# Kernel tuning notes

Measured on AMD Instinct MI355X. Metric: run time of the kernel, lower is better.

Reference implementation:

```python
import jax, jax.numpy as jnp
import numpy as np

B, T, D, H = 2, 2048, 2048, 16
HD = D // H
EPS = 1e-8
NEG = -1e9


def setup_inputs() -> dict:
    key = jax.random.key(0)
    ks = jax.random.split(key, 6)
    x = jax.random.normal(ks[0], (B, T, D), dtype=jnp.float32)
    # additive causal mask, broadcast over [B, H, T, T]
    causal = jnp.tril(jnp.ones((T, T), dtype=bool))
    attn_mask = jnp.where(causal, 0.0, NEG).astype(jnp.float32)[None, None]
    s = 1.0 / np.sqrt(D)
    w_norm = jnp.ones((D,), dtype=jnp.float32)
    wq = jax.random.normal(ks[1], (D, D), dtype=jnp.float32) * s
    wk = jax.random.normal(ks[2], (D, D), dtype=jnp.float32) * s
    wv = jax.random.normal(ks[3], (D, D), dtype=jnp.float32) * s
    wo = jax.random.normal(ks[4], (D, D), dtype=jnp.float32) * s
    return {"x": x, "attn_mask": attn_mask, "w_norm": w_norm,
            "wq": wq, "wk": wk, "wv": wv, "wo": wo}


def _rmsnorm(x, w):
    # norm = ||x||_2 * D^-0.5 ; out = w * x / (norm + eps)  (eps outside, as in source)
    norm = jnp.sqrt(jnp.sum(x * x, axis=-1, keepdims=True)) * (x.shape[-1] ** -0.5)
    return w * x / (norm + EPS)


def reference(x, attn_mask, w_norm, wq, wk, wv, wo):
    b, t, d = x.shape
    xn = _rmsnorm(x, w_norm)
    # Linear (no bias): y = x @ W^T ; split into heads -> [B, H, T, HD]
    def proj(w):
        return jnp.einsum('btd,ed->bte', xn, w).reshape(b, t, H, HD).transpose(0, 2, 1, 3)
    q, k, v = proj(wq), proj(wk), proj(wv)
    scale = HD ** -0.5
    w_scores = jnp.einsum('bhqd,bhkd->bhqk', q, k) * scale + attn_mask
    p = jax.nn.softmax(w_scores, axis=-1)
    out = jnp.einsum('bhqk,bhkd->bhqd', p, v)
    out = out.transpose(0, 2, 1, 3).reshape(b, t, d)
    return jnp.einsum('btd,ed->bte', out, wo)
```

## Files before the change

### kernel.cpp

```cpp
#include <hip/hip_runtime.h>
#include <stdint.h>

#define TT 2048
#define DD 2048
#define NHH 16
#define HDD 128
#define BTT 4096

typedef __attribute__((ext_vector_type(8))) short bf16x8;
typedef __attribute__((ext_vector_type(4))) float f32x4;

#define MF(a, b, c) __builtin_amdgcn_mfma_f32_16x16x32_bf16(a, b, c, 0, 0, 0)

__device__ __forceinline__ unsigned short f2bf(float f) {
    union { float f; uint32_t u; } v; v.f = f;
    uint32_t u = v.u;
    u += 0x7fffu + ((u >> 16) & 1u);
    return (unsigned short)(u >> 16);
}

__device__ __forceinline__ void gld16(const unsigned short* g, unsigned short* l) {
    __builtin_amdgcn_global_load_lds(
        (const __attribute__((address_space(1))) unsigned int*)g,
        (__attribute__((address_space(3))) unsigned int*)l, 16, 0, 0);
}

__global__ __launch_bounds__(256) void convert_w(const float* __restrict__ wq,
                                                 const float* __restrict__ wk,
                                                 const float* __restrict__ wv,
                                                 const float* __restrict__ wo,
                                                 unsigned short* __restrict__ out) {
    size_t gid = (size_t)blockIdx.x * 256 + threadIdx.x;
    size_t base = gid * 8;
    int which = (int)(base >> 22);
    const float* src = which == 0 ? wq : which == 1 ? wk : which == 2 ? wv : wo;
    size_t off = base & 4194303u;
    float4 a = ((const float4*)(src + off))[0];
    float4 b = ((const float4*)(src + off))[1];
    union { unsigned short us[8]; uint4 v; } pk;
    pk.us[0] = f2bf(a.x); pk.us[1] = f2bf(a.y); pk.us[2] = f2bf(a.z); pk.us[3] = f2bf(a.w);
    pk.us[4] = f2bf(b.x); pk.us[5] = f2bf(b.y); pk.us[6] = f2bf(b.z); pk.us[7] = f2bf(b.w);
    *(uint4*)(out + base) = pk.v;
}

__global__ __launch_bounds__(256) void rmsnorm_k(const float* __restrict__ x,
                                                 const float* __restrict__ w,
                                                 unsigned short* __restrict__ xn) {
    const int row = blockIdx.x;
    const int tid = threadIdx.x;
    const float* xr = x + (size_t)row * DD;
    float4 a = ((const float4*)xr)[tid * 2];
    float4 b = ((const float4*)xr)[tid * 2 + 1];
    float ss = a.x*a.x + a.y*a.y + a.z*a.z + a.w*a.w
             + b.x*b.x + b.y*b.y + b.z*b.z + b.w*b.w;
    #pragma unroll
    for (int m = 1; m < 64; m <<= 1) ss += __shfl_xor(ss, m, 64);
    __shared__ float wss[4];
    if ((tid & 63) == 0) wss[tid >> 6] = ss;
    __syncthreads();
    float total = wss[0] + wss[1] + wss[2] + wss[3];
    float norm = sqrtf(total) * 0.022097086912079612f;
    float inv = 1.0f / (norm + 1e-8f);
    float4 wa = ((const float4*)w)[tid * 2];
    float4 wb = ((const float4*)w)[tid * 2 + 1];
    union { unsigned short us[8]; uint4 v; } pk;
    pk.us[0] = f2bf(wa.x * a.x * inv); pk.us[1] = f2bf(wa.y * a.y * inv);
    pk.us[2] = f2bf(wa.z * a.z * inv); pk.us[3] = f2bf(wa.w * a.w * inv);
    pk.us[4] = f2bf(wb.x * b.x * inv); pk.us[5] = f2bf(wb.y * b.y * inv);
    pk.us[6] = f2bf(wb.z * b.z * inv); pk.us[7] = f2bf(wb.w * b.w * inv);
    ((uint4*)(xn + (size_t)row * DD))[tid] = pk.v;
}

__device__ __forceinline__ void gemm256_core(const unsigned short* __restrict__ Ag,
                                             const unsigned short* __restrict__ Bg,
                                             unsigned short* lds, f32x4 acc[8][4]) {
    const int tid = threadIdx.x;
    const int wave = tid >> 6, lane = tid & 63;
    const int wm = wave >> 2, wn = wave & 3;
    const int l15 = lane & 15, lq = lane >> 4, r7 = l15 & 7;
    const int gr = lane >> 3;
    const size_t goff = (size_t)gr * DD + (size_t)((((lane & 7) ^ gr)) * 8);
    const int xk0 = (lq ^ r7) * 8;
    const int xk1 = ((4 + lq) ^ r7) * 8;
    const int aro = (wm * 128 + l15) * 64;
    const int bro = 16384 + (wn * 64 + l15) * 64;
    const int sw16 = wave * 16;

    #pragma unroll
    for (int c = 0; c < 2; c++) {
        gld16(Ag + (size_t)(sw16 + c * 8) * DD + goff,       lds + (sw16 + c * 8) * 64);
        gld16(Ag + (size_t)(128 + sw16 + c * 8) * DD + goff, lds + (128 + sw16 + c * 8) * 64);
        gld16(Bg + (size_t)(sw16 + c * 8) * DD + goff,       lds + 16384 + (sw16 + c * 8) * 64);
        gld16(Bg + (size_t)(128 + sw16 + c * 8) * DD + goff, lds + 16384 + (128 + sw16 + c * 8) * 64);
    }
    asm volatile("s_waitcnt vmcnt(0)" ::: "memory");
    __builtin_amdgcn_sched_barrier(0);
    __builtin_amdgcn_s_barrier();

    for (int kt = 0; kt < DD / 64; kt++) {
        const int cur = (kt & 1) << 15;
        const int nxt = cur ^ 32768;
        const bool hn = (kt + 1 < DD / 64);
        const int kn = (kt + 1) * 64;
        const unsigned short* ac = lds + cur + aro;
        const unsigned short* bc = lds + cur + bro;
        bf16x8 af[4][2], bA[2][2], bB[2][2];

        #pragma unroll
        for (int m = 0; m < 4; m++) {
            af[m][0] = *(const bf16x8*)(ac + m * 1024 + xk0);
            af[m][1] = *(const bf16x8*)(ac + m * 1024 + xk1);
        }
        #pragma unroll
        for (int n = 0; n < 2; n++) {
            bA[n][0] = *(const bf16x8*)(bc + n * 1024 + xk0);
            bA[n][1] = *(const bf16x8*)(bc + n * 1024 + xk1);
        }
        if (hn) {
            gld16(Ag + (size_t)(sw16 + 0) * DD + kn + goff, lds + nxt + (sw16 + 0) * 64);
            gld16(Ag + (size_t)(sw16 + 8) * DD + kn + goff, lds + nxt + (sw16 + 8) * 64);
        }
        __builtin_amdgcn_s_barrier();
        asm volatile("s_waitcnt lgkmcnt(0)" ::: "memory");
        __builtin_amdgcn_sched_barrier(0);
        __builtin_amdgcn_s_setprio(1);
        #pragma unroll
        for (int m = 0; m < 4; m++)
            #pragma unroll
            for (int n = 0; n < 2; n++) {
                acc[m][n] = MF(af[m][0], bA[n][0], acc[m][n]);
                acc[m][n] = MF(af[m][1], bA[n][1], acc[m][n]);
            }
        __builtin_amdgcn_s_setprio(0);
        __builtin_amdgcn_s_barrier();

        #pragma unroll
        for (int n = 0; n < 2; n++) {
            bB[n][0] = *(const bf16x8*)(bc + (2 + n) * 1024 + xk0);
            bB[n][1] = *(const bf16x8*)(bc + (2 + n) * 1024 + xk1);
        }
        if (hn) {
            gld16(Ag + (size_t)(128 + sw16 + 0) * DD + kn + goff, lds + nxt + (128 + sw16 + 0) * 64);
            gld16(Ag + (size_t)(128 + sw16 + 8) * DD + kn + goff, lds + nxt + (128 + sw16 + 8) * 64);
        }
        __builtin_amdgcn_s_barrier();
        asm volatile("s_waitcnt lgkmcnt(0)" ::: "memory");
        __builtin_amdgcn_sched_barrier(0);
        __builtin_amdgcn_s_setprio(1);
        #pragma unroll
        for (int m = 0; m < 4; m++)
            #pragma unroll
            for (int n = 0; n < 2; n++) {
                acc[m][2 + n] = MF(af[m][0], bB[n][0], acc[m][2 + n]);
                acc[m][2 + n] = MF(af[m][1], bB[n][1], acc[m][2 + n]);
            }
        __builtin_amdgcn_s_setprio(0);
        __builtin_amdgcn_s_barrier();

        #pragma unroll
        for (int m = 0; m < 4; m++) {
            af[m][0] = *(const bf16x8*)(ac + (4 + m) * 1024 + xk0);
            af[m][1] = *(const bf16x8*)(ac + (4 + m) * 1024 + xk1);
        }
        if (hn) {
            gld16(Bg + (size_t)(sw16 + 0) * DD + kn + goff, lds + nxt + 16384 + (sw16 + 0) * 64);
            gld16(Bg + (size_t)(sw16 + 8) * DD + kn + goff, lds + nxt + 16384 + (sw16 + 8) * 64);
        }
        __builtin_amdgcn_s_barrier();
        asm volatile("s_waitcnt lgkmcnt(0)" ::: "memory");
        __builtin_amdgcn_sched_barrier(0);
        __builtin_amdgcn_s_setprio(1);
        #pragma unroll
        for (int m = 0; m < 4; m++)
            #pragma unroll
            for (int n = 0; n < 2; n++) {
                acc[4 + m][n] = MF(af[m][0], bA[n][0], acc[4 + m][n]);
                acc[4 + m][n] = MF(af[m][1], bA[n][1], acc[4 + m][n]);
            }
        __builtin_amdgcn_s_setprio(0);
        __builtin_amdgcn_s_barrier();

        if (hn) {
            gld16(Bg + (size_t)(128 + sw16 + 0) * DD + kn + goff, lds + nxt + 16384 + (128 + sw16 + 0) * 64);
            gld16(Bg + (size_t)(128 + sw16 + 8) * DD + kn + goff, lds + nxt + 16384 + (128 + sw16 + 8) * 64);
        }
        __builtin_amdgcn_s_barrier();
        __builtin_amdgcn_s_setprio(1);
        #pragma unroll
        for (int m = 0; m < 4; m++)
            #pragma unroll
            for (int n = 0; n < 2; n++) {
                acc[4 + m][2 + n] = MF(af[m][0], bB[n][0], acc[4 + m][2 + n]);
                acc[4 + m][2 + n] = MF(af[m][1], bB[n][1], acc[4 + m][2 + n]);
            }
        __builtin_amdgcn_s_setprio(0);
        asm volatile("s_waitcnt vmcnt(0)" ::: "memory");
        __builtin_amdgcn_sched_barrier(0);
        __builtin_amdgcn_s_barrier();
    }
}

__global__ __launch_bounds__(512, 2) void gemm_qkv(const unsigned short* __restrict__ A,
                                                   const unsigned short* __restrict__ W3,
                                                   unsigned short* __restrict__ O3) {
    __shared__ __align__(16) unsigned short lds[65536];
    const int nwg = 384;
    const int orig = blockIdx.y * 16 + blockIdx.x;
    const int id = (orig & 7) * (nwg / 8) + (orig >> 3);
    const int bx = id & 15, byy = id >> 4;
    const int which = byy >> 3;
    const unsigned short* Bw = W3 + (size_t)which * DD * DD;
    unsigned short* C = O3 + (size_t)which * BTT * DD;
    const int m0 = bx * 256, n0 = (byy & 7) * 256;
    const f32x4 zf = {0.f, 0.f, 0.f, 0.f};
    f32x4 acc[8][4];
    #pragma unroll
    for (int m = 0; m < 8; m++)
        #pragma unroll
        for (int n = 0; n < 4; n++) acc[m][n] = zf;
    gemm256_core(A + (size_t)m0 * DD, Bw + (size_t)n0 * DD, lds, acc);
    const int wave = threadIdx.x >> 6, lane = threadIdx.x & 63;
    const int wm = wave >> 2, wn = wave & 3;
    const int l15 = lane & 15, lq = lane >> 4;
    #pragma unroll
    for (int m = 0; m < 8; m++) {
        const int row = m0 + wm * 128 + m * 16 + lq * 4;
        #pragma unroll
        for (int n = 0; n < 4; n++) {
            const int col = n0 + wn * 64 + n * 16 + l15;
            #pragma unroll
            for (int r = 0; r < 4; r++)
                C[(size_t)(row + r) * DD + col] = f2bf(acc[m][n][r]);
        }
    }
}

__global__ __launch_bounds__(512, 2) void gemm_out(const unsigned short* __restrict__ A,
                                                   const unsigned short* __restrict__ Bw,
                                                   float* __restrict__ C) {
    __shared__ __align__(16) unsigned short lds[65536];
    const int nwg = 128;
    const int orig = blockIdx.y * 16 + blockIdx.x;
    const int id = (orig & 7) * (nwg / 8) + (orig >> 3);
    const int bx = id & 15, byy = id >> 4;
    const int m0 = bx * 256, n0 = byy * 256;
    const f32x4 zf = {0.f, 0.f, 0.f, 0.f};
    f32x4 acc[8][4];
    #pragma unroll
    for (int m = 0; m < 8; m++)
        #pragma unroll
        for (int n = 0; n < 4; n++) acc[m][n] = zf;
    gemm256_core(A + (size_t)m0 * DD, Bw + (size_t)n0 * DD, lds, acc);
    const int wave = threadIdx.x >> 6, lane = threadIdx.x & 63;
    const int wm = wave >> 2, wn = wave & 3;
    const int l15 = lane & 15, lq = lane >> 4;
    #pragma unroll
    for (int m = 0; m < 8; m++) {
        const int row = m0 + wm * 128 + m * 16 + lq * 4;
        #pragma unroll
        for (int n = 0; n < 4; n++) {
            const int col = n0 + wn * 64 + n * 16 + l15;
            #pragma unroll
            for (int r = 0; r < 4; r++)
                C[(size_t)(row + r) * DD + col] = acc[m][n][r];
        }
    }
}

__global__ __launch_bounds__(256) void attn_fused(const unsigned short* __restrict__ q,
                                                  const unsigned short* __restrict__ k,
                                                  const unsigned short* __restrict__ v,
                                                  unsigned short* __restrict__ o) {
    constexpr int LKK = 136;
    constexpr int LPP = 72;
    __shared__ __align__(16) unsigned short Ks[2][64 * LKK];
    __shared__ __align__(16) unsigned short Vts[128 * 64];
    __shared__ __align__(16) unsigned short Ps[4 * 16 * LPP];
    const int h = blockIdx.y, b = blockIdx.z;
    const int tid = threadIdx.x, wave = tid >> 6, lane = tid & 63;
    const int l15 = lane & 15, lq = lane >> 4;
    const size_t rowbase = (size_t)b * TT;
    const int hcol = h * HDD;
    const float scale = 0.08838834764831845f;
    unsigned short* Pw = Ps + wave * 16 * LPP;
    const f32x4 zf = {0.f, 0.f, 0.f, 0.f};

    uint4 kr0, kr1, kr2, kr3, vr0, vr1, vr2, vr3;
    const int sidx = tid * 8;
    const int srr = sidx >> 7;
    const int sc  = sidx & 127;
    const int swz = ((sc >> 3) & 7) << 3;
    const int srs0 = (srr +  0) ^ swz;
    const int srs1 = (srr + 16) ^ swz;
    const int srs2 = (srr + 32) ^ swz;
    const int srs3 = (srr + 48) ^ swz;

    for (int half = 0; half < 2; half++) {
        const int qj = (half == 0) ? blockIdx.x : 31 - blockIdx.x;
        const int qt0 = qj * 64;
        bf16x8 aq[4];
        {
            const unsigned short* qrp = q + (rowbase + qt0 + wave * 16 + l15) * DD + hcol;
            #pragma unroll
            for (int kk = 0; kk < 4; kk++)
                aq[kk] = *(const bf16x8*)(qrp + kk * 32 + lq * 8);
        }
        f32x4 acc_o[8];
        #pragma unroll
        for (int jh = 0; jh < 8; jh++) acc_o[jh] = zf;
        float m_i[4], l_i[4];
        #pragma unroll
        for (int r = 0; r < 4; r++) { m_i[r] = -1e30f; l_i[r] = 0.f; }
        const int qp0 = qt0 + wave * 16 + lq * 4;
        const int nkt = qj + 1;

        __syncthreads();
        {
            const unsigned short* kg = k + rowbase * DD + hcol;
            const unsigned short* vg = v + rowbase * DD + hcol;
            kr0 = *(const uint4*)(kg + (size_t)(srr +  0) * DD + sc);
            kr1 = *(const uint4*)(kg + (size_t)(srr + 16) * DD + sc);
            kr2 = *(const uint4*)(kg + (size_t)(srr + 32) * DD + sc);
            kr3 = *(const uint4*)(kg + (size_t)(srr + 48) * DD + sc);
            vr0 = *(const uint4*)(vg + (size_t)(srr +  0) * DD + sc);
            vr1 = *(const uint4*)(vg + (size_t)(srr + 16) * DD + sc);
            vr2 = *(const uint4*)(vg + (size_t)(srr + 32) * DD + sc);
            vr3 = *(const uint4*)(vg + (size_t)(srr + 48) * DD + sc);
            unsigned short* ksb = &Ks[0][0];
            *(uint4*)(ksb + (srr +  0) * LKK + sc) = kr0;
            *(uint4*)(ksb + (srr + 16) * LKK + sc) = kr1;
            *(uint4*)(ksb + (srr + 32) * LKK + sc) = kr2;
            *(uint4*)(ksb + (srr + 48) * LKK + sc) = kr3;
            if (nkt > 1) {
                const unsigned short* kg1 = k + (rowbase + 64) * DD + hcol;
                kr0 = *(const uint4*)(kg1 + (size_t)(srr +  0) * DD + sc);
                kr1 = *(const uint4*)(kg1 + (size_t)(srr + 16) * DD + sc);
                kr2 = *(const uint4*)(kg1 + (size_t)(srr + 32) * DD + sc);
                kr3 = *(const uint4*)(kg1 + (size_t)(srr + 48) * DD + sc);
            }
        }

        for (int kt = 0; kt < nkt; kt++) {
            const int cur = kt & 1;
            __syncthreads();
            {
                const unsigned short* d0 = (const unsigned short*)&vr0;
                const unsigned short* d1 = (const unsigned short*)&vr1;
                const unsigned short* d2 = (const unsigned short*)&vr2;
                const unsigned short* d3 = (const unsigned short*)&vr3;
                #pragma unroll
                for (int jj = 0; jj < 8; jj++) {
                    Vts[(sc + jj) * 64 + srs0] = d0[jj];
                    Vts[(sc + jj) * 64 + srs1] = d1[jj];
                    Vts[(sc + jj) * 64 + srs2] = d2[jj];
                    Vts[(sc + jj) * 64 + srs3] = d3[jj];
                }
            }
            if (kt + 1 < nkt) {
                unsigned short* ksb = &Ks[cur ^ 1][0];
                *(uint4*)(ksb + (srr +  0) * LKK + sc) = kr0;
                *(uint4*)(ksb + (srr + 16) * LKK + sc) = kr1;
                *(uint4*)(ksb + (srr + 32) * LKK + sc) = kr2;
                *(uint4*)(ksb + (srr + 48) * LKK + sc) = kr3;
            }
            if (kt + 2 < nkt) {
                const unsigned short* kg = k + (rowbase + (kt + 2) * 64) * DD + hcol;
                kr0 = *(const uint4*)(kg + (size_t)(srr +  0) * DD + sc);
                kr1 = *(const uint4*)(kg + (size_t)(srr + 16) * DD + sc);
                kr2 = *(const uint4*)(kg + (size_t)(srr + 32) * DD + sc);
                kr3 = *(const uint4*)(kg + (size_t)(srr + 48) * DD + sc);
            }
            if (kt + 1 < nkt) {
                const unsigned short* vg = v + (rowbase + (kt + 1) * 64) * DD + hcol;
                vr0 = *(const uint4*)(vg + (size_t)(srr +  0) * DD + sc);
                vr1 = *(const uint4*)(vg + (size_t)(srr + 16) * DD + sc);
                vr2 = *(const uint4*)(vg + (size_t)(srr + 32) * DD + sc);
                vr3 = *(const uint4*)(vg + (size_t)(srr + 48) * DD + sc);
            }
            const unsigned short* ksc = &Ks[cur][0];
            f32x4 accs[4];
            #pragma unroll
            for (int j = 0; j < 4; j++) accs[j] = zf;
            __builtin_amdgcn_s_setprio(1);
            #pragma unroll
            for (int j = 0; j < 4; j++)
                #pragma unroll
                for (int kk = 0; kk < 4; kk++) {
                    bf16x8 bk = *(const bf16x8*)(&ksc[(j * 16 + l15) * LKK + kk * 32 + lq * 8]);
                    accs[j] = MF(aq[kk], bk, accs[j]);
                }
            __builtin_amdgcn_s_setprio(0);
            const int kbase = kt * 64;
            float rowmax[4] = {-1e30f, -1e30f, -1e30f, -1e30f};
            #pragma unroll
            for (int j = 0; j < 4; j++) {
                const int kp = kbase + j * 16 + l15;
                #pragma unroll
                for (int r = 0; r < 4; r++) {
                    float s = accs[j][r] * scale;
                    s = (kp > qp0 + r) ? -1e30f : s;
                    accs[j][r] = s;
                    rowmax[r] = fmaxf(rowmax[r], s);
                }
            }
            #pragma unroll
            for (int r = 0; r < 4; r++) {
                float mx = rowmax[r];
                mx = fmaxf(mx, __shfl_xor(mx, 1, 64));
                mx = fmaxf(mx, __shfl_xor(mx, 2, 64));
                mx = fmaxf(mx, __shfl_xor(mx, 4, 64));
                mx = fmaxf(mx, __shfl_xor(mx, 8, 64));
                float m_new = fmaxf(m_i[r], mx);
                float al = __expf(m_i[r] - m_new);
                m_i[r] = m_new;
                l_i[r] *= al;
                #pragma unroll
                for (int jh = 0; jh < 8; jh++) acc_o[jh][r] *= al;
            }
            float rowsum[4] = {0.f, 0.f, 0.f, 0.f};
            #pragma unroll
            for (int j = 0; j < 4; j++)
                #pragma unroll
                for (int r = 0; r < 4; r++) {
                    float p = __expf(accs[j][r] - m_i[r]);
                    rowsum[r] += p;
                    Pw[(lq * 4 + r) * LPP + j * 16 + l15] = f2bf(p);
                }
            #pragma unroll
            for (int r = 0; r < 4; r++) {
                float s = rowsum[r];
                s += __shfl_xor(s, 1, 64);
                s += __shfl_xor(s, 2, 64);
                s += __shfl_xor(s, 4, 64);
                s += __shfl_xor(s, 8, 64);
                l_i[r] += s;
            }
            __syncthreads();
            bf16x8 ap[2];
            #pragma unroll
            for (int kk = 0; kk < 2; kk++)
                ap[kk] = *(const bf16x8*)(&Pw[l15 * LPP + kk * 32 + lq * 8]);
            __builtin_amdgcn_s_setprio(1);
            #pragma unroll
            for (int jh = 0; jh < 8; jh++) {
                const int hd = jh * 16 + l15;
                const int vswz = ((hd >> 3) & 7) << 3;
                #pragma unroll
                for (int kk = 0; kk < 2; kk++) {
                    bf16x8 bv = *(const bf16x8*)(&Vts[hd * 64 + ((kk * 32 + lq * 8) ^ vswz)]);
                    acc_o[jh] = MF(ap[kk], bv, acc_o[jh]);
                }
            }
            __builtin_amdgcn_s_setprio(0);
        }
        #pragma unroll
        for (int jh = 0; jh < 8; jh++) {
            const int col = hcol + jh * 16 + l15;
            #pragma unroll
            for (int r = 0; r < 4; r++)
                o[(rowbase + qp0 + r) * DD + col] = f2bf(acc_o[jh][r] * (1.0f / l_i[r]));
        }
    }
}

extern "C" void kernel_launch(void* const* d_in, const int* in_sizes, int n_in,
                              void* d_out, int out_size, void* d_ws, size_t ws_size,
                              hipStream_t stream) {
    const float* x      = (const float*)d_in[0];
    const float* w_norm = (const float*)d_in[2];
    const float* wq     = (const float*)d_in[3];
    const float* wk     = (const float*)d_in[4];
    const float* wv     = (const float*)d_in[5];
    const float* wo     = (const float*)d_in[6];

    unsigned short* wbf = (unsigned short*)d_ws;
    unsigned short* xn  = wbf + (size_t)4 * DD * DD;
    unsigned short* qb  = xn + (size_t)BTT * DD;
    unsigned short* kb  = qb + (size_t)BTT * DD;
    unsigned short* vb  = kb + (size_t)BTT * DD;
    unsigned short* ab  = vb + (size_t)BTT * DD;

    convert_w<<<8192, 256, 0, stream>>>(wq, wk, wv, wo, wbf);
    rmsnorm_k<<<BTT, 256, 0, stream>>>(x, w_norm, xn);
    dim3 gqkv(16, 24);
    gemm_qkv<<<gqkv, 512, 0, stream>>>(xn, wbf, qb);
    dim3 gattn(16, NHH, 2);
    attn_fused<<<gattn, 256, 0, stream>>>(qb, kb, vb, ab);
    dim3 gout(16, 8);
    gemm_out<<<gout, 512, 0, stream>>>(ab, wbf + (size_t)3 * DD * DD, (float*)d_out);
}
```

Baseline: 445.8 us.

## Shrink projection GEMM tiles to 128x256 to double workgroup count

The shared GEMM core now computes 128x256 output tiles instead of 256x256, with a smaller double-buffered LDS footprint. Each K-step issues all A/B loads for the next stage in one phase and runs two MFMA phases instead of four. The QKV and output GEMMs launch twice as many workgroups with remapped swizzled tile indices. The aim is to fill the 256 CUs better (gemm_out previously had only 128 blocks), at the cost of lower arithmetic intensity per tile and more global/L2 traffic.

```diff
diff --git a/kernel.cpp b/kernel.cpp
--- a/kernel.cpp
+++ b/kernel.cpp
@@ -71,45 +71,47 @@
     ((uint4*)(xn + (size_t)row * DD))[tid] = pk.v;
 }
 
-__device__ __forceinline__ void gemm256_core(const unsigned short* __restrict__ Ag,
-                                             const unsigned short* __restrict__ Bg,
-                                             unsigned short* lds, f32x4 acc[8][4]) {
+__device__ __forceinline__ void gemm128x256_core(const unsigned short* __restrict__ Ag,
+                                                 const unsigned short* __restrict__ Bg,
+                                                 unsigned short* lds, f32x4 acc[4][4]) {
     const int tid = threadIdx.x;
     const int wave = tid >> 6, lane = tid & 63;
     const int wm = wave >> 2, wn = wave & 3;
     const int l15 = lane & 15, lq = lane >> 4, r7 = l15 & 7;
     const int gr = lane >> 3;
-    const size_t goff = (size_t)gr * DD + (size_t)((((lane & 7) ^ gr)) * 8);
+    const size_t goff = (size_t)gr * DD + (size_t)(((lane & 7) ^ gr) * 8);
     const int xk0 = (lq ^ r7) * 8;
     const int xk1 = ((4 + lq) ^ r7) * 8;
-    const int aro = (wm * 128 + l15) * 64;
-    const int bro = 16384 + (wn * 64 + l15) * 64;
-    const int sw16 = wave * 16;
-
-    #pragma unroll
-    for (int c = 0; c < 2; c++) {
-        gld16(Ag + (size_t)(sw16 + c * 8) * DD + goff,       lds + (sw16 + c * 8) * 64);
-        gld16(Ag + (size_t)(128 + sw16 + c * 8) * DD + goff, lds + (128 + sw16 + c * 8) * 64);
-        gld16(Bg + (size_t)(sw16 + c * 8) * DD + goff,       lds + 16384 + (sw16 + c * 8) * 64);
-        gld16(Bg + (size_t)(128 + sw16 + c * 8) * DD + goff, lds + 16384 + (128 + sw16 + c * 8) * 64);
-    }
+    const int aro = (wm * 64 + l15) * 64;
+    const int bro = 8192 + (wn * 64 + l15) * 64;
+    const int swA = wave * 16;
+    const int swB = wave * 32;
+
+    #pragma unroll
+    for (int c = 0; c < 2; c++)
+        gld16(Ag + (size_t)(swA + c * 8) * DD + goff, lds + (swA + c * 8) * 64);
+    #pragma unroll
+    for (int c = 0; c < 4; c++)
+        gld16(Bg + (size_t)(swB + c * 8) * DD + goff, lds + 8192 + (swB + c * 8) * 64);
     asm volatile("s_waitcnt vmcnt(0)" ::: "memory");
     __builtin_amdgcn_sched_barrier(0);
     __builtin_amdgcn_s_barrier();
 
     for (int kt = 0; kt < DD / 64; kt++) {
-        const int cur = (kt & 1) << 15;
-        const int nxt = cur ^ 32768;
+        const int cur = (kt & 1) ? 24576 : 0;
+        const int nxt = 24576 - cur;
         const bool hn = (kt + 1 < DD / 64);
         const int kn = (kt + 1) * 64;
         const unsigned short* ac = lds + cur + aro;
         const unsigned short* bc = lds + cur + bro;
-        bf16x8 af[4][2], bA[2][2], bB[2][2];
-
-        #pragma unroll
-        for (int m = 0; m < 4; m++) {
-            af[m][0] = *(const bf16x8*)(ac + m * 1024 + xk0);
-            af[m][1] = *(const bf16x8*)(ac + m * 1024 + xk1);
+        bf16x8 afA[2][2], afB[2][2], bA[2][2], bB[2][2];
+
+        #pragma unroll
+        for (int m = 0; m < 2; m++) {
+            afA[m][0] = *(const bf16x8*)(ac + m * 1024 + xk0);
+            afA[m][1] = *(const bf16x8*)(ac + m * 1024 + xk1);
+            afB[m][0] = *(const bf16x8*)(ac + (2 + m) * 1024 + xk0);
+            afB[m][1] = *(const bf16x8*)(ac + (2 + m) * 1024 + xk1);
         }
         #pragma unroll
         for (int n = 0; n < 2; n++) {
@@ -117,19 +119,27 @@
             bA[n][1] = *(const bf16x8*)(bc + n * 1024 + xk1);
         }
         if (hn) {
-            gld16(Ag + (size_t)(sw16 + 0) * DD + kn + goff, lds + nxt + (sw16 + 0) * 64);
-            gld16(Ag + (size_t)(sw16 + 8) * DD + kn + goff, lds + nxt + (sw16 + 8) * 64);
+            #pragma unroll
+            for (int c = 0; c < 2; c++)
+                gld16(Ag + (size_t)(swA + c * 8) * DD + kn + goff,
+                      lds + nxt + (swA + c * 8) * 64);
+            #pragma unroll
+            for (int c = 0; c < 4; c++)
+                gld16(Bg + (size_t)(swB + c * 8) * DD + kn + goff,
+                      lds + nxt + 8192 + (swB + c * 8) * 64);
         }
         __builtin_amdgcn_s_barrier();
         asm volatile("s_waitcnt lgkmcnt(0)" ::: "memory");
         __builtin_amdgcn_sched_barrier(0);
         __builtin_amdgcn_s_setprio(1);
         #pragma unroll
-        for (int m = 0; m < 4; m++)
+        for (int m = 0; m < 2; m++)
             #pragma unroll
             for (int n = 0; n < 2; n++) {
-                acc[m][n] = MF(af[m][0], bA[n][0], acc[m][n]);
-                acc[m][n] = MF(af[m][1], bA[n][1], acc[m][n]);
+                acc[m][n]     = MF(afA[m][0], bA[n][0], acc[m][n]);
+                acc[m][n]     = MF(afA[m][1], bA[n][1], acc[m][n]);
+                acc[2 + m][n] = MF(afB[m][0], bA[n][0], acc[2 + m][n]);
+                acc[2 + m][n] = MF(afB[m][1], bA[n][1], acc[2 + m][n]);
             }
         __builtin_amdgcn_s_setprio(0);
         __builtin_amdgcn_s_barrier();
@@ -138,60 +148,19 @@
         for (int n = 0; n < 2; n++) {
             bB[n][0] = *(const bf16x8*)(bc + (2 + n) * 1024 + xk0);
             bB[n][1] = *(const bf16x8*)(bc + (2 + n) * 1024 + xk1);
-        }
-        if (hn) {
-            gld16(Ag + (size_t)(128 + sw16 + 0) * DD + kn + goff, lds + nxt + (128 + sw16 + 0) * 64);
-            gld16(Ag + (size_t)(128 + sw16 + 8) * DD + kn + goff, lds + nxt + (128 + sw16 + 8) * 64);
         }
         __builtin_amdgcn_s_barrier();
         asm volatile("s_waitcnt lgkmcnt(0)" ::: "memory");
         __builtin_amdgcn_sched_barrier(0);
         __builtin_amdgcn_s_setprio(1);
         #pragma unroll
-        for (int m = 0; m < 4; m++)
+        for (int m = 0; m < 2; m++)
             #pragma unroll
             for (int n = 0; n < 2; n++) {
-                acc[m][2 + n] = MF(af[m][0], bB[n][0], acc[m][2 + n]);
-                acc[m][2 + n] = MF(af[m][1], bB[n][1], acc[m][2 + n]);
-            }
-        __builtin_amdgcn_s_setprio(0);
-        __builtin_amdgcn_s_barrier();
-
-        #pragma unroll
-        for (int m = 0; m < 4; m++) {
-            af[m][0] = *(const bf16x8*)(ac + (4 + m) * 1024 + xk0);
-            af[m][1] = *(const bf16x8*)(ac + (4 + m) * 1024 + xk1);
-        }
-        if (hn) {
-            gld16(Bg + (size_t)(sw16 + 0) * DD + kn + goff, lds + nxt + 16384 + (sw16 + 0) * 64);
-            gld16(Bg + (size_t)(sw16 + 8) * DD + kn + goff, lds + nxt + 16384 + (sw16 + 8) * 64);
-        }
-        __builtin_amdgcn_s_barrier();
-        asm volatile("s_waitcnt lgkmcnt(0)" ::: "memory");
-        __builtin_amdgcn_sched_barrier(0);
-        __builtin_amdgcn_s_setprio(1);
-        #pragma unroll
-        for (int m = 0; m < 4; m++)
-            #pragma unroll
-            for (int n = 0; n < 2; n++) {
-                acc[4 + m][n] = MF(af[m][0], bA[n][0], acc[4 + m][n]);
-                acc[4 + m][n] = MF(af[m][1], bA[n][1], acc[4 + m][n]);
-            }
-        __builtin_amdgcn_s_setprio(0);
-        __builtin_amdgcn_s_barrier();
-
-        if (hn) {
-            gld16(Bg + (size_t)(128 + sw16 + 0) * DD + kn + goff, lds + nxt + 16384 + (128 + sw16 + 0) * 64);
-            gld16(Bg + (size_t)(128 + sw16 + 8) * DD + kn + goff, lds + nxt + 16384 + (128 + sw16 + 8) * 64);
-        }
-        __builtin_amdgcn_s_barrier();
-        __builtin_amdgcn_s_setprio(1);
-        #pragma unroll
-        for (int m = 0; m < 4; m++)
-            #pragma unroll
-            for (int n = 0; n < 2; n++) {
-                acc[4 + m][2 + n] = MF(af[m][0], bB[n][0], acc[4 + m][2 + n]);
-                acc[4 + m][2 + n] = MF(af[m][1], bB[n][1], acc[4 + m][2 + n]);
+                acc[m][2 + n]     = MF(afA[m][0], bB[n][0], acc[m][2 + n]);
+                acc[m][2 + n]     = MF(afA[m][1], bB[n][1], acc[m][2 + n]);
+                acc[2 + m][2 + n] = MF(afB[m][0], bB[n][0], acc[2 + m][2 + n]);
+                acc[2 + m][2 + n] = MF(afB[m][1], bB[n][1], acc[2 + m][2 + n]);
             }
         __builtin_amdgcn_s_setprio(0);
         asm volatile("s_waitcnt vmcnt(0)" ::: "memory");
@@ -203,28 +172,28 @@
 __global__ __launch_bounds__(512, 2) void gemm_qkv(const unsigned short* __restrict__ A,
                                                    const unsigned short* __restrict__ W3,
                                                    unsigned short* __restrict__ O3) {
-    __shared__ __align__(16) unsigned short lds[65536];
-    const int nwg = 384;
-    const int orig = blockIdx.y * 16 + blockIdx.x;
-    const int id = (orig & 7) * (nwg / 8) + (orig >> 3);
-    const int bx = id & 15, byy = id >> 4;
-    const int which = byy >> 3;
+    __shared__ __align__(16) unsigned short lds[49152];
+    const int orig = blockIdx.y * 32 + blockIdx.x;
+    const int id = (orig & 7) * 96 + (orig >> 3);
+    const int which = id >> 8;
+    const int rem = id & 255;
+    const int bn = rem >> 5, bm = rem & 31;
     const unsigned short* Bw = W3 + (size_t)which * DD * DD;
     unsigned short* C = O3 + (size_t)which * BTT * DD;
-    const int m0 = bx * 256, n0 = (byy & 7) * 256;
+    const int m0 = bm * 128, n0 = bn * 256;
     const f32x4 zf = {0.f, 0.f, 0.f, 0.f};
-    f32x4 acc[8][4];
-    #pragma unroll
-    for (int m = 0; m < 8; m++)
+    f32x4 acc[4][4];
+    #pragma unroll
+    for (int m = 0; m < 4; m++)
         #pragma unroll
         for (int n = 0; n < 4; n++) acc[m][n] = zf;
-    gemm256_core(A + (size_t)m0 * DD, Bw + (size_t)n0 * DD, lds, acc);
+    gemm128x256_core(A + (size_t)m0 * DD, Bw + (size_t)n0 * DD, lds, acc);
     const int wave = threadIdx.x >> 6, lane = threadIdx.x & 63;
     const int wm = wave >> 2, wn = wave & 3;
     const int l15 = lane & 15, lq = lane >> 4;
     #pragma unroll
-    for (int m = 0; m < 8; m++) {
-        const int row = m0 + wm * 128 + m * 16 + lq * 4;
+    for (int m = 0; m < 4; m++) {
+        const int row = m0 + wm * 64 + m * 16 + lq * 4;
         #pragma unroll
         for (int n = 0; n < 4; n++) {
             const int col = n0 + wn * 64 + n * 16 + l15;
@@ -238,25 +207,24 @@
 __global__ __launch_bounds__(512, 2) void gemm_out(const unsigned short* __restrict__ A,
                                                    const unsigned short* __restrict__ Bw,
                                                    float* __restrict__ C) {
-    __shared__ __align__(16) unsigned short lds[65536];
-    const int nwg = 128;
-    const int orig = blockIdx.y * 16 + blockIdx.x;
-    const int id = (orig & 7) * (nwg / 8) + (orig >> 3);
-    const int bx = id & 15, byy = id >> 4;
-    const int m0 = bx * 256, n0 = byy * 256;
+    __shared__ __align__(16) unsigned short lds[49152];
+    const int orig = blockIdx.y * 32 + blockIdx.x;
+    const int id = (orig & 7) * 32 + (orig >> 3);
+    const int bn = id >> 5, bm = id & 31;
+    const int m0 = bm * 128, n0 = bn * 256;
     const f32x4 zf = {0.f, 0.f, 0.f, 0.f};
-    f32x4 acc[8][4];
-    #pragma unroll
-    for (int m = 0; m < 8; m++)
+    f32x4 acc[4][4];
+    #pragma unroll
+    for (int m = 0; m < 4; m++)
         #pragma unroll
         for (int n = 0; n < 4; n++) acc[m][n] = zf;
-    gemm256_core(A + (size_t)m0 * DD, Bw + (size_t)n0 * DD, lds, acc);
+    gemm128x256_core(A + (size_t)m0 * DD, Bw + (size_t)n0 * DD, lds, acc);
     const int wave = threadIdx.x >> 6, lane = threadIdx.x & 63;
     const int wm = wave >> 2, wn = wave & 3;
     const int l15 = lane & 15, lq = lane >> 4;
     #pragma unroll
-    for (int m = 0; m < 8; m++) {
-        const int row = m0 + wm * 128 + m * 16 + lq * 4;
+    for (int m = 0; m < 4; m++) {
+        const int row = m0 + wm * 64 + m * 16 + lq * 4;
         #pragma unroll
         for (int n = 0; n < 4; n++) {
             const int col = n0 + wn * 64 + n * 16 + l15;
@@ -482,10 +450,10 @@
 
     convert_w<<<8192, 256, 0, stream>>>(wq, wk, wv, wo, wbf);
     rmsnorm_k<<<BTT, 256, 0, stream>>>(x, w_norm, xn);
-    dim3 gqkv(16, 24);
+    dim3 gqkv(32, 24);
     gemm_qkv<<<gqkv, 512, 0, stream>>>(xn, wbf, qb);
     dim3 gattn(16, NHH, 2);
     attn_fused<<<gattn, 256, 0, stream>>>(qb, kb, vb, ab);
-    dim3 gout(16, 8);
+    dim3 gout(32, 8);
     gemm_out<<<gout, 512, 0, stream>>>(ab, wbf + (size_t)3 * DD * DD, (float*)d_out);
 }
```

Result: faster. 429.7 us (-3.6%).
